# Optimization experiments

Hardware: AMD Instinct MI355X
Metric: run time of the kernel (lower is better)

## Reference

```python
import jax, jax.numpy as jnp
import numpy as np

NUM_HEADS = 16
HIDDEN = 1024
HEAD_DIM = HIDDEN // NUM_HEADS


def setup_inputs() -> dict:
    key = jax.random.key(0)
    ks = jax.random.split(key, 9)
    B, S = 2, 2048
    scale = 1.0 / np.sqrt(HIDDEN)
    x = jax.random.normal(ks[0], (B, S, HIDDEN), dtype=jnp.float32)
    Wq = jax.random.uniform(ks[1], (HIDDEN, HIDDEN), jnp.float32, -scale, scale)
    bq = jax.random.uniform(ks[2], (HIDDEN,), jnp.float32, -scale, scale)
    Wk = jax.random.uniform(ks[3], (HIDDEN, HIDDEN), jnp.float32, -scale, scale)
    bk = jax.random.uniform(ks[4], (HIDDEN,), jnp.float32, -scale, scale)
    Wv = jax.random.uniform(ks[5], (HIDDEN, HIDDEN), jnp.float32, -scale, scale)
    bv = jax.random.uniform(ks[6], (HIDDEN,), jnp.float32, -scale, scale)
    Wo = jax.random.uniform(ks[7], (HIDDEN, HIDDEN), jnp.float32, -scale, scale)
    bo = jax.random.uniform(ks[8], (HIDDEN,), jnp.float32, -scale, scale)
    return {"x": x, "Wq": Wq, "bq": bq, "Wk": Wk, "bk": bk,
            "Wv": Wv, "bv": bv, "Wo": Wo, "bo": bo}


def reference(x, Wq, bq, Wk, bk, Wv, bv, Wo, bo):
    B, S, _ = x.shape
    H, D = NUM_HEADS, HEAD_DIM
    # projections (torch Linear: x @ W^T + b)
    q = (x @ Wq.T + bq).reshape(B, S, H, D).transpose(0, 2, 1, 3)  # [B,H,S,D]
    k = (x @ Wk.T + bk).reshape(B, S, H, D).transpose(0, 2, 1, 3)
    v = (x @ Wv.T + bv).reshape(B, S, H, D).transpose(0, 2, 1, 3)
    scores = jnp.einsum("bhqd,bhkd->bhqk", q, k) / jnp.sqrt(jnp.float32(D))
    causal = jnp.tril(jnp.ones((S, S), dtype=bool))  # True = keep
    scores = jnp.where(causal, scores, -jnp.inf)
    weights = jax.nn.softmax(scores, axis=-1)
    out = jnp.einsum("bhqk,bhkd->bhqd", weights, v)  # [B,H,S,D]
    out = out.transpose(0, 2, 1, 3).reshape(B, S, H * D)
    return out @ Wo.T + bo
```

## Files before the change

kernel.cpp:

```cpp
#include <hip/hip_runtime.h>
#include <stdint.h>


#define HIDDEN 1024
#define NH 16
#define HD 64
#define BATCH 2
#define SEQ 2048

typedef unsigned short u16;
typedef unsigned int u32;
typedef __attribute__((ext_vector_type(8))) short short8;
typedef __attribute__((ext_vector_type(4))) float f32x4;

typedef const __attribute__((address_space(1))) u32 gu32;
typedef __attribute__((address_space(3))) u32 lu32;

__device__ __forceinline__ u16 f2bf(float f) {
    u32 u = __float_as_uint(f);
    return (u16)((u + 0x7FFFu + ((u >> 16) & 1u)) >> 16);
}

__global__ void cvt_all(const float* __restrict__ x, const float* __restrict__ Wq,
                        const float* __restrict__ Wk, const float* __restrict__ Wv,
                        const float* __restrict__ Wo, u16* __restrict__ xb,
                        u16* __restrict__ wqb, u16* __restrict__ wkb,
                        u16* __restrict__ wvb, u16* __restrict__ wob) {
    const int blk = blockIdx.x;
    const float* src; u16* dst; int base;
    if (blk < 2048)      { src = x;  dst = xb;  base = blk; }
    else if (blk < 2560) { src = Wq; dst = wqb; base = blk - 2048; }
    else if (blk < 3072) { src = Wk; dst = wkb; base = blk - 2560; }
    else if (blk < 3584) { src = Wv; dst = wvb; base = blk - 3072; }
    else                 { src = Wo; dst = wob; base = blk - 3584; }
    const int i = base * 256 + threadIdx.x;
    float4 a = ((const float4*)src)[2 * i];
    float4 b = ((const float4*)src)[2 * i + 1];
    union { u16 h[8]; uint4 v; } o;
    o.h[0] = f2bf(a.x); o.h[1] = f2bf(a.y); o.h[2] = f2bf(a.z); o.h[3] = f2bf(a.w);
    o.h[4] = f2bf(b.x); o.h[5] = f2bf(b.y); o.h[6] = f2bf(b.z); o.h[7] = f2bf(b.w);
    ((uint4*)dst)[i] = o.v;
}

__device__ __forceinline__ void stage16(const u16* __restrict__ G, int grow0,
                                        int k0, u16* lds, int rbase, int lane) {
    const int sr = lane >> 2;
    const int lc = (lane & 3) ^ (sr & 3);
    const u16* g = G + (size_t)(grow0 + rbase + sr) * 1024 + k0 + lc * 8;
    __builtin_amdgcn_global_load_lds((gu32*)g, (lu32*)(lds + rbase * 32), 16, 0, 0);
}

__launch_bounds__(256, 3)
__global__ void gemm_qkv(const u16* __restrict__ A, const u16* __restrict__ Wqb,
                         const u16* __restrict__ Wkb, const u16* __restrict__ Wvb,
                         const float* __restrict__ bq, const float* __restrict__ bk,
                         const float* __restrict__ bv, u16* __restrict__ Qo,
                         u16* __restrict__ Ko, u16* __restrict__ Vo) {
    __shared__ u16 As[2][128 * 32];
    __shared__ u16 Bs[2][128 * 32];
    const int which = blockIdx.x >> 3;
    const int n0 = (blockIdx.x & 7) * 128;
    const int m0 = blockIdx.y * 128;
    const u16* Wt = (which == 0) ? Wqb : (which == 1) ? Wkb : Wvb;
    const float* bias = (which == 0) ? bq : (which == 1) ? bk : bv;
    u16* out = (which == 0) ? Qo : (which == 1) ? Ko : Vo;
    const float oscale = (which == 0) ? 0.18033688011112042f : 1.0f;
    const int t = threadIdx.x;
    const int lane = t & 63, w = t >> 6, quad = lane >> 4, lm = lane & 15;
    const int wm = (w & 1) * 64, wn = (w >> 1) * 64;

    f32x4 acc[4][4] = {};

    auto stage = [&](int k0, int buf) {
        stage16(A, m0, k0, As[buf], w * 32, lane);
        stage16(A, m0, k0, As[buf], w * 32 + 16, lane);
        stage16(Wt, n0, k0, Bs[buf], w * 32, lane);
        stage16(Wt, n0, k0, Bs[buf], w * 32 + 16, lane);
    };

    stage(0, 0);
    __syncthreads();
    for (int k0 = 0; k0 < 1024; k0 += 32) {
        const int cur = (k0 >> 5) & 1;
        if (k0 + 32 < 1024) stage(k0 + 32, cur ^ 1);
        short8 af[4], bf[4];
        const int sw = (quad ^ (lm & 3)) * 8;
#pragma unroll
        for (int mi = 0; mi < 4; mi++)
            af[mi] = *(const short8*)(&As[cur][(wm + mi * 16 + lm) * 32] + sw);
#pragma unroll
        for (int ni = 0; ni < 4; ni++)
            bf[ni] = *(const short8*)(&Bs[cur][(wn + ni * 16 + lm) * 32] + sw);
#pragma unroll
        for (int mi = 0; mi < 4; mi++)
#pragma unroll
            for (int ni = 0; ni < 4; ni++)
                acc[mi][ni] = __builtin_amdgcn_mfma_f32_16x16x32_bf16(
                    af[mi], bf[ni], acc[mi][ni], 0, 0, 0);
        __syncthreads();
    }

    if (which == 2) {
        u16* Tw = ((w < 2) ? (u16*)As : (u16*)Bs) + (w & 1) * 4096;
#pragma unroll
        for (int ni = 0; ni < 4; ni++) {
            const int n_loc = ni * 16 + lm;
            const float bv_ = bias[n0 + wn + n_loc];
#pragma unroll
            for (int mi = 0; mi < 4; mi++)
#pragma unroll
                for (int r = 0; r < 4; r++) {
                    const int m_loc = mi * 16 + quad * 4 + r;
                    Tw[n_loc * 64 + (((m_loc >> 3) ^ (n_loc & 7)) * 8) + (m_loc & 7)] =
                        f2bf(acc[mi][ni][r] + bv_);
                }
        }
        const int hh = (n0 + wn) >> 6;
        const int mg = m0 + wm;
        const int bb = mg >> 11, s0 = mg & 2047;
        u16* outp = out + ((size_t)(bb * NH + hh) * HD) * SEQ;
        const int cm = lane & 7;
#pragma unroll
        for (int i = 0; i < 8; i++) {
            const int n_loc = i * 8 + (lane >> 3);
            short8 v = *(const short8*)(Tw + n_loc * 64 + ((cm ^ (n_loc & 7)) * 8));
            *(short8*)(outp + (size_t)n_loc * SEQ + s0 + cm * 8) = v;
        }
    } else {
#pragma unroll
        for (int ni = 0; ni < 4; ni++) {
            const int n = n0 + wn + ni * 16 + lm;
            const float bv_ = bias[n];
            const int h = n >> 6, d = n & 63;
#pragma unroll
            for (int mi = 0; mi < 4; mi++)
#pragma unroll
                for (int r = 0; r < 4; r++) {
                    const int m = m0 + wm + mi * 16 + quad * 4 + r;
                    const int b = m >> 11, s = m & 2047;
                    out[(((size_t)(b * NH + h) * SEQ + s) * HD) + d] =
                        f2bf((acc[mi][ni][r] + bv_) * oscale);
                }
        }
    }
}

__launch_bounds__(256, 2)
__global__ void gemm_out(const u16* __restrict__ A, const u16* __restrict__ Wt,
                         const float* __restrict__ bias, float* __restrict__ out) {
    __shared__ u16 As[2][64 * 32];
    __shared__ u16 Bs[2][128 * 32];
    const int n0 = blockIdx.x * 128;
    const int m0 = blockIdx.y * 64;
    const int t = threadIdx.x;
    const int lane = t & 63, w = t >> 6, quad = lane >> 4, lm = lane & 15;
    const int wm = (w & 1) * 32, wn = (w >> 1) * 64;

    f32x4 acc[2][4] = {};

    auto stage = [&](int k0, int buf) {
        stage16(A, m0, k0, As[buf], w * 16, lane);
        stage16(Wt, n0, k0, Bs[buf], w * 32, lane);
        stage16(Wt, n0, k0, Bs[buf], w * 32 + 16, lane);
    };

    stage(0, 0);
    __syncthreads();
    for (int k0 = 0; k0 < 1024; k0 += 32) {
        const int cur = (k0 >> 5) & 1;
        if (k0 + 32 < 1024) stage(k0 + 32, cur ^ 1);
        short8 af[2], bf[4];
        const int sw = (quad ^ (lm & 3)) * 8;
#pragma unroll
        for (int mi = 0; mi < 2; mi++)
            af[mi] = *(const short8*)(&As[cur][(wm + mi * 16 + lm) * 32] + sw);
#pragma unroll
        for (int ni = 0; ni < 4; ni++)
            bf[ni] = *(const short8*)(&Bs[cur][(wn + ni * 16 + lm) * 32] + sw);
#pragma unroll
        for (int mi = 0; mi < 2; mi++)
#pragma unroll
            for (int ni = 0; ni < 4; ni++)
                acc[mi][ni] = __builtin_amdgcn_mfma_f32_16x16x32_bf16(
                    af[mi], bf[ni], acc[mi][ni], 0, 0, 0);
        __syncthreads();
    }

#pragma unroll
    for (int ni = 0; ni < 4; ni++) {
        const int n = n0 + wn + ni * 16 + lm;
        const float bv_ = bias[n];
#pragma unroll
        for (int mi = 0; mi < 2; mi++)
#pragma unroll
            for (int r = 0; r < 4; r++) {
                const int m = m0 + wm + mi * 16 + quad * 4 + r;
                out[(size_t)m * 1024 + n] = acc[mi][ni][r] + bv_;
            }
    }
}

__launch_bounds__(256, 4)
__global__ void attn_kernel(const u16* __restrict__ Q, const u16* __restrict__ K,
                            const u16* __restrict__ Vt, u16* __restrict__ Out) {
    __shared__ u16 Ks[2][64 * 64];
    __shared__ u16 Vs[2][64 * 64];
    __shared__ u16 Ps[4 * 16 * 64];
    const int t = threadIdx.x;
    const int lane = t & 63, w = t >> 6, quad = lane >> 4, lm = lane & 15;
    const int i = blockIdx.x >> 5;
    const int qt = (i < 16) ? (31 - i) : (i - 16);
    const int bh = blockIdx.x & 31;
    const int b = bh >> 4, h = bh & 15;
    const size_t base = (size_t)(b * NH + h) * SEQ * HD;
    const u16* Qg = Q + base;
    const u16* Kg = K + base;
    const u16* Vg = Vt + base;
    const int q0 = qt * 64 + w * 16;
    const int nk = qt + 1;

    short8 qf[2];
#pragma unroll
    for (int kk = 0; kk < 2; kk++)
        qf[kk] = *(const short8*)(Qg + (size_t)(q0 + lm) * HD + kk * 32 + quad * 8);

    f32x4 oacc[4] = {};
    f32x4 lacc = {};
    short8 ones;
#pragma unroll
    for (int j = 0; j < 8; j++) ones[j] = (short)0x3F80;

    u16* Pw = Ps + w * 16 * 64;

    const int srow = (lane >> 3);
    const int schunk = (lane & 7) ^ srow;
    auto stage_kv = [&](int kt, int buf) {
#pragma unroll
        for (int j = 0; j < 2; j++) {
            const int row = w * 16 + j * 8 + srow;
            const u16* gk = Kg + (size_t)(kt * 64 + row) * HD + schunk * 8;
            const u16* gv = Vg + (size_t)row * SEQ + kt * 64 + schunk * 8;
            __builtin_amdgcn_global_load_lds((gu32*)gk, (lu32*)(&Ks[buf][(w * 16 + j * 8) * 64]), 16, 0, 0);
            __builtin_amdgcn_global_load_lds((gu32*)gv, (lu32*)(&Vs[buf][(w * 16 + j * 8) * 64]), 16, 0, 0);
        }
    };

    auto compute_step = [&](const u16* Kc, const u16* Vc, int kt_) {
        f32x4 sacc[4];
        __builtin_amdgcn_s_setprio(1);
#pragma unroll
        for (int n = 0; n < 4; n++) {
            const int r = n * 16 + lm;
            const u16* rowp = Kc + r * 64;
            short8 kf0 = *(const short8*)(rowp + ((quad ^ (r & 7)) * 8));
            short8 kf1 = *(const short8*)(rowp + (((quad + 4) ^ (r & 7)) * 8));
            f32x4 a = {};
            a = __builtin_amdgcn_mfma_f32_16x16x32_bf16(kf0, qf[0], a, 0, 0, 0);
            a = __builtin_amdgcn_mfma_f32_16x16x32_bf16(kf1, qf[1], a, 0, 0, 0);
            sacc[n] = a;
        }
        __builtin_amdgcn_s_setprio(0);
        if (kt_ == qt) {
#pragma unroll
            for (int n = 0; n < 4; n++)
#pragma unroll
                for (int r = 0; r < 4; r++)
                    if (n * 16 + quad * 4 + r > w * 16 + lm)
                        sacc[n][r] = -__builtin_inff();
        }
        {
            const int q = lm;
            const int co = (quad & 1) * 4;
#pragma unroll
            for (int n = 0; n < 4; n++) {
                u32 e0 = __float_as_uint(exp2f(sacc[n][0]));
                u32 e1 = __float_as_uint(exp2f(sacc[n][1]));
                u32 e2 = __float_as_uint(exp2f(sacc[n][2]));
                u32 e3 = __float_as_uint(exp2f(sacc[n][3]));
                uint2 pk;
                pk.x = (e0 >> 16) | (e1 & 0xFFFF0000u);
                pk.y = (e2 >> 16) | (e3 & 0xFFFF0000u);
                const int chunk = (n * 2 + (quad >> 1)) ^ (q & 7);
                *(uint2*)(Pw + q * 64 + chunk * 8 + co) = pk;
            }
        }
        short8 pf[2];
#pragma unroll
        for (int k4 = 0; k4 < 2; k4++)
            pf[k4] = *(const short8*)(Pw + lm * 64 + (((k4 * 4 + quad) ^ (lm & 7)) * 8));
        __builtin_amdgcn_s_setprio(1);
#pragma unroll
        for (int n = 0; n < 4; n++) {
            const int r = n * 16 + lm;
            const u16* rowp = Vc + r * 64;
#pragma unroll
            for (int k4 = 0; k4 < 2; k4++) {
                short8 vf = *(const short8*)(rowp + (((k4 * 4 + quad) ^ (r & 7)) * 8));
                oacc[n] = __builtin_amdgcn_mfma_f32_16x16x32_bf16(pf[k4], vf, oacc[n], 0, 0, 0);
            }
        }
#pragma unroll
        for (int k4 = 0; k4 < 2; k4++)
            lacc = __builtin_amdgcn_mfma_f32_16x16x32_bf16(pf[k4], ones, lacc, 0, 0, 0);
        __builtin_amdgcn_s_setprio(0);
    };

    stage_kv(0, 0);
    __syncthreads();

    for (int kt = 0; kt < nk; kt++) {
        const int cur = kt & 1;
        if (kt + 1 < nk) stage_kv(kt + 1, cur ^ 1);
        compute_step(Ks[cur], Vs[cur], kt);
        __syncthreads();
    }

    float inv[4];
#pragma unroll
    for (int r = 0; r < 4; r++) inv[r] = 1.0f / lacc[r];
#pragma unroll
    for (int n = 0; n < 4; n++)
#pragma unroll
        for (int r = 0; r < 4; r++) {
            const int qq = q0 + quad * 4 + r;
            Out[(size_t)(b * SEQ + qq) * HIDDEN + h * HD + n * 16 + lm] =
                f2bf(oacc[n][r] * inv[r]);
        }
}

extern "C" void kernel_launch(void* const* d_in, const int* in_sizes, int n_in,
                              void* d_out, int out_size, void* d_ws, size_t ws_size,
                              hipStream_t stream) {
    const float* x  = (const float*)d_in[0];
    const float* Wq = (const float*)d_in[1];
    const float* bq = (const float*)d_in[2];
    const float* Wk = (const float*)d_in[3];
    const float* bk = (const float*)d_in[4];
    const float* Wv = (const float*)d_in[5];
    const float* bv = (const float*)d_in[6];
    const float* Wo = (const float*)d_in[7];
    const float* bo = (const float*)d_in[8];
    float* out = (float*)d_out;

    char* ws = (char*)d_ws;
    const size_t SZ_X = (size_t)4096 * 1024 * 2;
    const size_t SZ_W = (size_t)1024 * 1024 * 2;
    u16* xb    = (u16*)(ws);
    u16* wqb   = (u16*)(ws + SZ_X);
    u16* wkb   = (u16*)(ws + SZ_X + SZ_W);
    u16* wvb   = (u16*)(ws + SZ_X + 2 * SZ_W);
    u16* wob   = (u16*)(ws + SZ_X + 3 * SZ_W);
    u16* Qb    = (u16*)(ws + SZ_X + 4 * SZ_W);
    u16* Kb    = (u16*)(ws + 2 * SZ_X + 4 * SZ_W);
    u16* Vtb   = (u16*)(ws + 3 * SZ_X + 4 * SZ_W);
    u16* attnb = (u16*)(ws + 4 * SZ_X + 4 * SZ_W);

    cvt_all<<<4096, 256, 0, stream>>>(x, Wq, Wk, Wv, Wo, xb, wqb, wkb, wvb, wob);
    gemm_qkv<<<dim3(24, 32), 256, 0, stream>>>(xb, wqb, wkb, wvb, bq, bk, bv, Qb, Kb, Vtb);
    attn_kernel<<<BATCH * NH * (SEQ / 64), 256, 0, stream>>>(Qb, Kb, Vtb, attnb);
    gemm_out<<<dim3(8, 64), 256, 0, stream>>>(attnb, wob, bo, out);
}
```

Before: 189.5 us.

## Pair causal q-tiles per block and software-pipeline QK ahead of PV

Each attention block now handles two query tiles (qt and 31-qt) in sequence, giving every block the same amount of causal work and halving the grid to 512 blocks. Inside the loop, K is prefetched two tiles ahead and the QK^T MFMA for the next tile is issued before the PV MFMA of the current tile. The goal is to overlap the softmax/LDS work with matrix ops and to remove load imbalance. P packing also switches to the hardware v_cvt_pk_bf16_f32 instruction with a new 4-element LDS swizzle, which rounds instead of truncating and costs extra LDS reads.

```diff
diff --git a/kernel.cpp b/kernel.cpp
--- a/kernel.cpp
+++ b/kernel.cpp
@@ -208,124 +208,144 @@
     __shared__ u16 Ps[4 * 16 * 64];
     const int t = threadIdx.x;
     const int lane = t & 63, w = t >> 6, quad = lane >> 4, lm = lane & 15;
-    const int i = blockIdx.x >> 5;
-    const int qt = (i < 16) ? (31 - i) : (i - 16);
+    const int pairIdx = blockIdx.x >> 5;
     const int bh = blockIdx.x & 31;
     const int b = bh >> 4, h = bh & 15;
     const size_t base = (size_t)(b * NH + h) * SEQ * HD;
     const u16* Qg = Q + base;
     const u16* Kg = K + base;
     const u16* Vg = Vt + base;
-    const int q0 = qt * 64 + w * 16;
-    const int nk = qt + 1;
-
-    short8 qf[2];
-#pragma unroll
-    for (int kk = 0; kk < 2; kk++)
-        qf[kk] = *(const short8*)(Qg + (size_t)(q0 + lm) * HD + kk * 32 + quad * 8);
-
-    f32x4 oacc[4] = {};
-    f32x4 lacc = {};
-    short8 ones;
-#pragma unroll
-    for (int j = 0; j < 8; j++) ones[j] = (short)0x3F80;
 
     u16* Pw = Ps + w * 16 * 64;
 
     const int srow = (lane >> 3);
     const int schunk = (lane & 7) ^ srow;
-    auto stage_kv = [&](int kt, int buf) {
+    auto stage_k = [&](int kt, int buf) {
 #pragma unroll
         for (int j = 0; j < 2; j++) {
             const int row = w * 16 + j * 8 + srow;
             const u16* gk = Kg + (size_t)(kt * 64 + row) * HD + schunk * 8;
+            __builtin_amdgcn_global_load_lds((gu32*)gk, (lu32*)(&Ks[buf][(w * 16 + j * 8) * 64]), 16, 0, 0);
+        }
+    };
+    auto stage_v = [&](int kt, int buf) {
+#pragma unroll
+        for (int j = 0; j < 2; j++) {
+            const int row = w * 16 + j * 8 + srow;
             const u16* gv = Vg + (size_t)row * SEQ + kt * 64 + schunk * 8;
-            __builtin_amdgcn_global_load_lds((gu32*)gk, (lu32*)(&Ks[buf][(w * 16 + j * 8) * 64]), 16, 0, 0);
             __builtin_amdgcn_global_load_lds((gu32*)gv, (lu32*)(&Vs[buf][(w * 16 + j * 8) * 64]), 16, 0, 0);
         }
     };
 
-    auto compute_step = [&](const u16* Kc, const u16* Vc, int kt_) {
+    short8 ones;
+#pragma unroll
+    for (int j = 0; j < 8; j++) ones[j] = (short)0x3F80;
+
+#pragma unroll 1
+    for (int half = 0; half < 2; half++) {
+        const int qt = half ? pairIdx : (31 - pairIdx);
+        const int q0 = qt * 64 + w * 16;
+        const int nk = qt + 1;
+
+        if (half) __syncthreads();
+
+        short8 qf[2];
+#pragma unroll
+        for (int kk = 0; kk < 2; kk++)
+            qf[kk] = *(const short8*)(Qg + (size_t)(q0 + lm) * HD + kk * 32 + quad * 8);
+
+        f32x4 oacc[4] = {};
+        f32x4 lacc = {};
         f32x4 sacc[4];
-        __builtin_amdgcn_s_setprio(1);
-#pragma unroll
-        for (int n = 0; n < 4; n++) {
-            const int r = n * 16 + lm;
-            const u16* rowp = Kc + r * 64;
-            short8 kf0 = *(const short8*)(rowp + ((quad ^ (r & 7)) * 8));
-            short8 kf1 = *(const short8*)(rowp + (((quad + 4) ^ (r & 7)) * 8));
-            f32x4 a = {};
-            a = __builtin_amdgcn_mfma_f32_16x16x32_bf16(kf0, qf[0], a, 0, 0, 0);
-            a = __builtin_amdgcn_mfma_f32_16x16x32_bf16(kf1, qf[1], a, 0, 0, 0);
-            sacc[n] = a;
-        }
-        __builtin_amdgcn_s_setprio(0);
-        if (kt_ == qt) {
-#pragma unroll
-            for (int n = 0; n < 4; n++)
-#pragma unroll
-                for (int r = 0; r < 4; r++)
-                    if (n * 16 + quad * 4 + r > w * 16 + lm)
-                        sacc[n][r] = -__builtin_inff();
-        }
-        {
-            const int q = lm;
-            const int co = (quad & 1) * 4;
+
+        auto qk_tile = [&](const u16* Kc) {
+            __builtin_amdgcn_s_setprio(1);
 #pragma unroll
             for (int n = 0; n < 4; n++) {
-                u32 e0 = __float_as_uint(exp2f(sacc[n][0]));
-                u32 e1 = __float_as_uint(exp2f(sacc[n][1]));
-                u32 e2 = __float_as_uint(exp2f(sacc[n][2]));
-                u32 e3 = __float_as_uint(exp2f(sacc[n][3]));
-                uint2 pk;
-                pk.x = (e0 >> 16) | (e1 & 0xFFFF0000u);
-                pk.y = (e2 >> 16) | (e3 & 0xFFFF0000u);
-                const int chunk = (n * 2 + (quad >> 1)) ^ (q & 7);
-                *(uint2*)(Pw + q * 64 + chunk * 8 + co) = pk;
-            }
-        }
-        short8 pf[2];
-#pragma unroll
-        for (int k4 = 0; k4 < 2; k4++)
-            pf[k4] = *(const short8*)(Pw + lm * 64 + (((k4 * 4 + quad) ^ (lm & 7)) * 8));
-        __builtin_amdgcn_s_setprio(1);
-#pragma unroll
-        for (int n = 0; n < 4; n++) {
-            const int r = n * 16 + lm;
-            const u16* rowp = Vc + r * 64;
+                const int r = n * 16 + lm;
+                const u16* rowp = Kc + r * 64;
+                short8 kf0 = *(const short8*)(rowp + ((quad ^ (r & 7)) * 8));
+                short8 kf1 = *(const short8*)(rowp + (((quad + 4) ^ (r & 7)) * 8));
+                f32x4 a = {};
+                a = __builtin_amdgcn_mfma_f32_16x16x32_bf16(kf0, qf[0], a, 0, 0, 0);
+                a = __builtin_amdgcn_mfma_f32_16x16x32_bf16(kf1, qf[1], a, 0, 0, 0);
+                sacc[n] = a;
+            }
+            __builtin_amdgcn_s_setprio(0);
+        };
+
+        stage_k(0, 0);
+        __syncthreads();
+        if (nk > 1) stage_k(1, 1);
+        stage_v(0, 0);
+        qk_tile(Ks[0]);
+        __syncthreads();
+
+        for (int kt = 0; kt < nk; kt++) {
+            const int kb = kt & 1;
+            if (kt + 2 < nk) stage_k(kt + 2, kb);
+            if (kt + 1 < nk) stage_v(kt + 1, kb ^ 1);
+
+            if (kt == qt) {
+#pragma unroll
+                for (int n = 0; n < 4; n++)
+#pragma unroll
+                    for (int r = 0; r < 4; r++)
+                        if (n * 16 + quad * 4 + r > w * 16 + lm)
+                            sacc[n][r] = -__builtin_inff();
+            }
+#pragma unroll
+            for (int n = 0; n < 4; n++) {
+                float e0 = exp2f(sacc[n][0]), e1 = exp2f(sacc[n][1]);
+                float e2 = exp2f(sacc[n][2]), e3 = exp2f(sacc[n][3]);
+                u32 lo, hi;
+                asm("v_cvt_pk_bf16_f32 %0, %1, %2" : "=v"(lo) : "v"(e0), "v"(e1));
+                asm("v_cvt_pk_bf16_f32 %0, %1, %2" : "=v"(hi) : "v"(e2), "v"(e3));
+                const int pslot = (n * 4 + quad) ^ lm;
+                *(uint2*)(Pw + lm * 64 + pslot * 4) = (uint2){lo, hi};
+            }
+            short8 pf[2];
 #pragma unroll
             for (int k4 = 0; k4 < 2; k4++) {
-                short8 vf = *(const short8*)(rowp + (((k4 * 4 + quad) ^ (r & 7)) * 8));
-                oacc[n] = __builtin_amdgcn_mfma_f32_16x16x32_bf16(pf[k4], vf, oacc[n], 0, 0, 0);
-            }
-        }
-#pragma unroll
-        for (int k4 = 0; k4 < 2; k4++)
-            lacc = __builtin_amdgcn_mfma_f32_16x16x32_bf16(pf[k4], ones, lacc, 0, 0, 0);
-        __builtin_amdgcn_s_setprio(0);
-    };
-
-    stage_kv(0, 0);
-    __syncthreads();
-
-    for (int kt = 0; kt < nk; kt++) {
-        const int cur = kt & 1;
-        if (kt + 1 < nk) stage_kv(kt + 1, cur ^ 1);
-        compute_step(Ks[cur], Vs[cur], kt);
-        __syncthreads();
-    }
-
-    float inv[4];
-#pragma unroll
-    for (int r = 0; r < 4; r++) inv[r] = 1.0f / lacc[r];
-#pragma unroll
-    for (int n = 0; n < 4; n++)
-#pragma unroll
-        for (int r = 0; r < 4; r++) {
-            const int qq = q0 + quad * 4 + r;
-            Out[(size_t)(b * SEQ + qq) * HIDDEN + h * HD + n * 16 + lm] =
-                f2bf(oacc[n][r] * inv[r]);
-        }
+                const int l0 = k4 * 8 + quad * 2;
+                uint2 a = *(const uint2*)(Pw + lm * 64 + ((l0 ^ lm) * 4));
+                uint2 c = *(const uint2*)(Pw + lm * 64 + (((l0 + 1) ^ lm) * 4));
+                union { short8 s; uint4 u; } m_;
+                m_.u = (uint4){a.x, a.y, c.x, c.y};
+                pf[k4] = m_.s;
+            }
+            if (kt + 1 < nk) qk_tile(Ks[kb ^ 1]);
+            __builtin_amdgcn_s_setprio(1);
+#pragma unroll
+            for (int n = 0; n < 4; n++) {
+                const int r = n * 16 + lm;
+                const u16* rowp = Vs[kb] + r * 64;
+#pragma unroll
+                for (int k4 = 0; k4 < 2; k4++) {
+                    short8 vf = *(const short8*)(rowp + (((k4 * 4 + quad) ^ (r & 7)) * 8));
+                    oacc[n] = __builtin_amdgcn_mfma_f32_16x16x32_bf16(pf[k4], vf, oacc[n], 0, 0, 0);
+                }
+            }
+#pragma unroll
+            for (int k4 = 0; k4 < 2; k4++)
+                lacc = __builtin_amdgcn_mfma_f32_16x16x32_bf16(pf[k4], ones, lacc, 0, 0, 0);
+            __builtin_amdgcn_s_setprio(0);
+
+            if (kt + 1 < nk) __syncthreads();
+        }
+
+        float inv[4];
+#pragma unroll
+        for (int r = 0; r < 4; r++) inv[r] = 1.0f / lacc[r];
+#pragma unroll
+        for (int n = 0; n < 4; n++)
+#pragma unroll
+            for (int r = 0; r < 4; r++) {
+                const int qq = q0 + quad * 4 + r;
+                Out[(size_t)(b * SEQ + qq) * HIDDEN + h * HD + n * 16 + lm] =
+                    f2bf(oacc[n][r] * inv[r]);
+            }
+    }
 }
 
 extern "C" void kernel_launch(void* const* d_in, const int* in_sizes, int n_in,
@@ -357,6 +377,6 @@
 
     cvt_all<<<4096, 256, 0, stream>>>(x, Wq, Wk, Wv, Wo, xb, wqb, wkb, wvb, wob);
     gemm_qkv<<<dim3(24, 32), 256, 0, stream>>>(xb, wqb, wkb, wvb, bq, bk, bv, Qb, Kb, Vtb);
-    attn_kernel<<<BATCH * NH * (SEQ / 64), 256, 0, stream>>>(Qb, Kb, Vtb, attnb);
+    attn_kernel<<<512, 256, 0, stream>>>(Qb, Kb, Vtb, attnb);
     gemm_out<<<dim3(8, 64), 256, 0, stream>>>(attnb, wob, bo, out);
 }
```

New measurement: 187.3 us. Within noise of the previous version (-1.2%).
